# Performance work log

Measured on AMD Instinct MI355X. Metric: run time of the kernel, lower is better.

The kernel has to match this reference:

```python
import jax, jax.numpy as jnp
import numpy as np

PI = np.pi


def _apply_1q(state, gate, wire, n):
    # state: [B, 2**n] complex64; gate: [2,2] (shared) or [B,2,2] (per-sample)
    # PennyLane convention: wire 0 is the most-significant bit of the state index.
    B = state.shape[0]
    left, right = 2 ** wire, 2 ** (n - wire - 1)
    s = state.reshape(B, left, 2, right)
    if gate.ndim == 2:
        s = jnp.einsum('kl,balr->bakr', gate, s)
    else:
        s = jnp.einsum('bkl,balr->bakr', gate, s)
    return s.reshape(B, -1)


def _apply_cz(state, wire, n):
    # CZ on (wire, wire+1): flip sign of |..11..> amplitudes
    B = state.shape[0]
    left, right = 2 ** wire, 2 ** (n - wire - 2)
    s = state.reshape(B, left, 2, 2, right)
    s = s.at[:, :, 1, 1, :].multiply(-1.0)
    return s.reshape(B, -1)


def _ry_batched(theta):
    # theta: [B] -> [B,2,2] complex RY(theta)
    h = 0.5 * theta
    c, s = jnp.cos(h), jnp.sin(h)
    g = jnp.stack([jnp.stack([c, -s], -1), jnp.stack([s, c], -1)], -2)
    return g.astype(jnp.complex64)


def _rot(phi, theta, omega):
    # Rot = RZ(omega) @ RY(theta) @ RZ(phi)
    c, s = jnp.cos(0.5 * theta), jnp.sin(0.5 * theta)
    e_mm = jnp.exp(-0.5j * (phi + omega))
    e_pm = jnp.exp(0.5j * (phi - omega))
    e_mp = jnp.exp(-0.5j * (phi - omega))
    e_pp = jnp.exp(0.5j * (phi + omega))
    g = jnp.stack([jnp.stack([e_mm * c, -e_pm * s]), jnp.stack([e_mp * s, e_pp * c])])
    return g.astype(jnp.complex64)


def _simulate(enc, weights):
    # enc: [B, n_qubits] in [-1,1]; weights: [n_layers, n_qubits, 3]
    n_layers, n, _ = weights.shape
    B = enc.shape[0]
    state = jnp.zeros((B, 2 ** n), jnp.complex64).at[:, 0].set(1.0)
    ry = [_ry_batched(enc[:, i] * PI) for i in range(n)]
    for l in range(n_layers):
        for i in range(n):
            state = _apply_1q(state, ry[i], i, n)
        for i in range(n):
            state = _apply_1q(state, _rot(weights[l, i, 0], weights[l, i, 1], weights[l, i, 2]), i, n)
        for i in range(n - 1):
            state = _apply_cz(state, i, n)
    for i in range(n):
        state = _apply_1q(state, ry[i], i, n)
    probs = state.real ** 2 + state.imag ** 2  # [B, 2**n]
    # <Z_i> = sum_k probs[k] * (-1)^bit_i(k), wire 0 = MSB
    bits = (jnp.arange(2 ** n)[None, :] >> (n - 1 - jnp.arange(n))[:, None]) & 1
    signs = (1 - 2 * bits).astype(probs.dtype)  # [n, 2**n]
    return probs @ signs.T  # [B, n]


def setup_inputs() -> dict:
    B, D, NQ, NL, NA = 32768, 16, 8, 4, 4
    key = jax.random.key(0)
    ks = jax.random.split(key, 6)

    def lin(k, o, i):
        b = 1.0 / np.sqrt(i)
        k1, k2 = jax.random.split(k)
        return (jax.random.uniform(k1, (o, i), jnp.float32, -b, b),
                jax.random.uniform(k2, (o,), jnp.float32, -b, b))

    enc_w1, enc_b1 = lin(ks[1], 8, D)
    enc_w2, enc_b2 = lin(ks[2], NQ, 8)
    dec_w1, dec_b1 = lin(ks[3], 8, NQ)
    dec_w2, dec_b2 = lin(ks[4], NA, 8)
    q_weights = jax.random.uniform(ks[5], (NL, NQ, 3), jnp.float32, 0.0, 2.0 * PI)
    x = jax.random.normal(ks[0], (B, D), jnp.float32)
    return {"x": x, "enc_w1": enc_w1, "enc_b1": enc_b1, "enc_w2": enc_w2, "enc_b2": enc_b2,
            "q_weights": q_weights, "dec_w1": dec_w1, "dec_b1": dec_b1, "dec_w2": dec_w2, "dec_b2": dec_b2}


def reference(x, enc_w1, enc_b1, enc_w2, enc_b2, q_weights, dec_w1, dec_b1, dec_w2, dec_b2):
    h = jax.nn.relu(x @ enc_w1.T + enc_b1)
    enc = jnp.tanh(h @ enc_w2.T + enc_b2)          # [B, n_qubits]
    q = _simulate(enc, q_weights)                  # [B, n_qubits] PauliZ expvals
    h2 = jax.nn.relu(q @ dec_w1.T + dec_b1)
    return h2 @ dec_w2.T + dec_b2                  # [B, n_actions]
```

## Files before the change

kernel.cpp:

```cpp
#include <hip/hip_runtime.h>
#include <math.h>


#define PI_F 3.14159265358979323846f

struct C2 { float re, im; };

__device__ __forceinline__ C2 cmul(C2 a, C2 b) {
    C2 r;
    r.re = fmaf(a.re, b.re, -a.im * b.im);
    r.im = fmaf(a.re, b.im,  a.im * b.re);
    return r;
}

__device__ __forceinline__ void cdot2(const C2& g, float ar, float ai,
                                      const C2& h, float br, float bi,
                                      float& outr, float& outi) {
    outr = fmaf(g.re, ar, fmaf(-g.im, ai, fmaf(h.re, br, -h.im * bi)));
    outi = fmaf(g.re, ai, fmaf( g.im, ar, fmaf(h.re, bi,  h.im * br)));
}

__device__ __forceinline__ void load_G(const float* __restrict__ c_lds, int g,
                                       float cc, float ss,
                                       C2& G00, C2& G01, C2& G10, C2& G11) {
    const float4* cp = (const float4*)(c_lds + 8 * g);
    float4 c0 = cp[0];
    float4 c1 = cp[1];
    G00.re = fmaf(c0.x, cc,  c0.z * ss);  G00.im = fmaf(c0.y, cc,  c0.w * ss);
    G01.re = fmaf(c0.z, cc, -c0.x * ss);  G01.im = fmaf(c0.w, cc, -c0.y * ss);
    G10.re = fmaf(c1.x, cc,  c1.z * ss);  G10.im = fmaf(c1.y, cc,  c1.w * ss);
    G11.re = fmaf(c1.z, cc, -c1.x * ss);  G11.im = fmaf(c1.w, cc, -c1.y * ss);
}

__device__ __forceinline__ void apply_gate16(int q, int lane,
                                             C2 G00, C2 G01, C2 G10, C2 G11,
                                             float sr[16], float si[16]) {
    if (q < 4) {
        const int sh = 3 - q;
        const int m = 1 << sh;
        const bool hi = (lane >> sh) & 1;
        C2 cS = hi ? G11 : G00;
        C2 cO = hi ? G10 : G01;
#pragma unroll
        for (int t = 0; t < 16; t++) {
            float pr = __shfl_xor(sr[t], m, 64);
            float pi = __shfl_xor(si[t], m, 64);
            float nr, ni;
            cdot2(cS, sr[t], si[t], cO, pr, pi, nr, ni);
            sr[t] = nr; si[t] = ni;
        }
    } else {
        const int st = 1 << (7 - q);
#pragma unroll
        for (int t = 0; t < 16; t++) {
            if ((t & st) == 0) {
                const int u = t + st;
                float ar = sr[t], ai = si[t], br = sr[u], bi = si[u];
                cdot2(G00, ar, ai, G01, br, bi, sr[t], si[t]);
                cdot2(G10, ar, ai, G11, br, bi, sr[u], si[u]);
            }
        }
    }
}

__device__ __constant__ const bool CZNEG[16] =
    { false,false,false,true,  false,false,true,false,
      false,false,false,true,  true, true, false,true };

__global__ __launch_bounds__(256) void qdqn_kernel(
    const float* __restrict__ x,
    const float* __restrict__ ew1, const float* __restrict__ eb1,
    const float* __restrict__ ew2, const float* __restrict__ eb2,
    const float* __restrict__ qw,
    const float* __restrict__ dw1, const float* __restrict__ db1,
    const float* __restrict__ dw2, const float* __restrict__ db2,
    float* __restrict__ out, int B, int NL) {
    __shared__ __align__(16) float c_lds[64 * 8];

    const int tid = threadIdx.x;
    const int n_gates = NL * 8;

    if (tid < n_gates) {
        const int g = tid;
        float phi = qw[3 * g + 0], th = qw[3 * g + 1], om = qw[3 * g + 2];
        float c = __cosf(0.5f * th), s = __sinf(0.5f * th);
        float A = 0.5f * (phi + om), Bb = 0.5f * (phi - om);
        float cA = __cosf(A), sA = __sinf(A), cB = __cosf(Bb), sB = __sinf(Bb);
        float* o = c_lds + 8 * g;
        o[0] =  cA * c;  o[1] = -sA * c;
        o[2] = -cB * s;  o[3] = -sB * s;
        o[4] =  cB * s;  o[5] = -sB * s;
        o[6] =  cA * c;  o[7] =  sA * c;
    }
    __syncthreads();

    const int wave = tid >> 6;
    const int lane = tid & 63;
    const int L = lane & 15;
    int s = (blockIdx.x * 4 + wave) * 4 + (lane >> 4);
    if (s >= B) s = B - 1;

    float xv[16];
    const float4* xp = (const float4*)(x + s * 16);
#pragma unroll
    for (int i = 0; i < 4; i++) {
        float4 v = xp[i];
        xv[4*i] = v.x; xv[4*i+1] = v.y; xv[4*i+2] = v.z; xv[4*i+3] = v.w;
    }
    float hbuf[8];
#pragma unroll
    for (int j = 0; j < 8; j++) {
        float a = eb1[j];
#pragma unroll
        for (int i = 0; i < 16; i++) a = fmaf(ew1[j * 16 + i], xv[i], a);
        hbuf[j] = fmaxf(a, 0.0f);
    }
    float cq[8], sq[8];
#pragma unroll
    for (int q = 0; q < 8; q++) {
        float a = eb2[q];
#pragma unroll
        for (int j = 0; j < 8; j++) a = fmaf(ew2[q * 8 + j], hbuf[j], a);
        float e = 1.0f - __fdividef(2.0f, __expf(2.0f * a) + 1.0f);
        float ang = e * (0.5f * PI_F);
        cq[q] = __cosf(ang);
        sq[q] = __sinf(ang);
    }

    {
    }
    const int L0 = L & 1, L1b = (L >> 1) & 1, L2b = (L >> 2) & 1, L3b = (L >> 3) & 1;
    const int cnt = (L3b & L2b) + (L2b & L1b) + (L1b & L0);
    const float mL = (cnt & 1) ? -1.0f : 1.0f;
    const float mH = L0 ? -mL : mL;

    float sr[16], si[16];
    {
        C2 P; P.re = 1.0f; P.im = 0.0f;
        C2 F[4][2];
#pragma unroll
        for (int q = 0; q < 8; q++) {
            C2 G00, G01, G10, G11;
            load_G(c_lds, q, cq[q], sq[q], G00, G01, G10, G11);
            if (q < 4) {
                const int sh = 3 - q;
                const bool hi = (lane >> sh) & 1;
                C2 f = hi ? G10 : G00;
                P = cmul(P, f);
            } else {
                F[q - 4][0] = G00;
                F[q - 4][1] = G10;
            }
        }
        C2 A0 = cmul(P, F[0][0]), A1 = cmul(P, F[0][1]);
        C2 Bv[4];
        Bv[0] = cmul(A0, F[1][0]); Bv[1] = cmul(A0, F[1][1]);
        Bv[2] = cmul(A1, F[1][0]); Bv[3] = cmul(A1, F[1][1]);
        C2 Cv[8];
#pragma unroll
        for (int i = 0; i < 8; i++) Cv[i] = cmul(Bv[i >> 1], F[2][i & 1]);
#pragma unroll
        for (int t = 0; t < 16; t++) {
            C2 v = cmul(Cv[t >> 1], F[3][t & 1]);
            float m = (t < 8) ? mL : mH;
            m = CZNEG[t] ? -m : m;
            sr[t] = v.re * m;
            si[t] = v.im * m;
        }
    }

    for (int l = 1; l < NL; l++) {
#pragma unroll
        for (int q = 0; q < 8; q++) {
            C2 G00, G01, G10, G11;
            load_G(c_lds, l * 8 + q, cq[q], sq[q], G00, G01, G10, G11);
            apply_gate16(q, lane, G00, G01, G10, G11, sr, si);
        }
#pragma unroll
        for (int t = 0; t < 16; t++) {
            float m = (t < 8) ? mL : mH;
            m = CZNEG[t] ? -m : m;
            sr[t] *= m; si[t] *= m;
        }
    }

#pragma unroll
    for (int q = 0; q < 8; q++) {
        const float c = cq[q], sv = sq[q];
        if (q < 4) {
            const int sh = 3 - q;
            const int m = 1 << sh;
            const bool hi = (lane >> sh) & 1;
            const float cO = hi ? sv : -sv;
#pragma unroll
            for (int t = 0; t < 16; t++) {
                float pr = __shfl_xor(sr[t], m, 64);
                float pi = __shfl_xor(si[t], m, 64);
                sr[t] = fmaf(c, sr[t], cO * pr);
                si[t] = fmaf(c, si[t], cO * pi);
            }
        } else {
            const int st = 1 << (7 - q);
#pragma unroll
            for (int t = 0; t < 16; t++) {
                if ((t & st) == 0) {
                    const int u = t + st;
                    float ar = sr[t], ai = si[t], br = sr[u], bi = si[u];
                    sr[t] = fmaf(c, ar, -sv * br); si[t] = fmaf(c, ai, -sv * bi);
                    sr[u] = fmaf(sv, ar,  c * br); si[u] = fmaf(sv, ai,  c * bi);
                }
            }
        }
    }

    float p[16];
#pragma unroll
    for (int t = 0; t < 16; t++) p[t] = fmaf(sr[t], sr[t], si[t] * si[t]);

    float e0 = p[0]+p[1],  e1 = p[2]+p[3],  e2 = p[4]+p[5],  e3 = p[6]+p[7];
    float e4 = p[8]+p[9],  e5 = p[10]+p[11], e6 = p[12]+p[13], e7 = p[14]+p[15];
    float q0 = e0+e1, q1 = e2+e3, q2 = e4+e5, q3 = e6+e7;
    float h0 = q0+q1, h1 = q2+q3;
    float sumP = h0 + h1;

    float z[8];
#pragma unroll
    for (int w = 0; w < 4; w++)
        z[w] = ((L >> (3 - w)) & 1) ? -sumP : sumP;
    z[4] = h0 - h1;
    z[5] = (q0 - q1) + (q2 - q3);
    z[6] = (e0 - e1) + (e2 - e3) + (e4 - e5) + (e6 - e7);
    z[7] = (p[0]-p[1]) + (p[2]-p[3]) + (p[4]-p[5]) + (p[6]-p[7])
         + (p[8]-p[9]) + (p[10]-p[11]) + (p[12]-p[13]) + (p[14]-p[15]);

#pragma unroll
    for (int m = 1; m < 16; m <<= 1) {
#pragma unroll
        for (int w = 0; w < 8; w++) z[w] += __shfl_xor(z[w], m, 64);
    }

    float h2[8];
#pragma unroll
    for (int j = 0; j < 8; j++) {
        float a = db1[j];
#pragma unroll
        for (int w = 0; w < 8; w++) a = fmaf(dw1[j * 8 + w], z[w], a);
        h2[j] = fmaxf(a, 0.0f);
    }
    if (L < 4) {
        float a = db2[L];
#pragma unroll
        for (int j = 0; j < 8; j++) a = fmaf(dw2[L * 8 + j], h2[j], a);
        out[s * 4 + L] = a;
    }
}

extern "C" void kernel_launch(void* const* d_in, const int* in_sizes, int n_in,
                              void* d_out, int out_size, void* d_ws, size_t ws_size,
                              hipStream_t stream) {
    const float* x   = (const float*)d_in[0];
    const float* ew1 = (const float*)d_in[1];
    const float* eb1 = (const float*)d_in[2];
    const float* ew2 = (const float*)d_in[3];
    const float* eb2 = (const float*)d_in[4];
    const float* qw  = (const float*)d_in[5];
    const float* dw1 = (const float*)d_in[6];
    const float* db1 = (const float*)d_in[7];
    const float* dw2 = (const float*)d_in[8];
    const float* db2 = (const float*)d_in[9];
    float* out = (float*)d_out;

    int B = in_sizes[0] / 16;
    int n_gates = in_sizes[5] / 3;
    int NL = n_gates / 8;

    int blocks = (B + 15) / 16;
    qdqn_kernel<<<blocks, 256, 0, stream>>>(x, ew1, eb1, ew2, eb2, qw,
                                            dw1, db1, dw2, db2, out, B, NL);
}
```

Measured before the change: 139.0 us.

## Use DPP/swizzle lane exchanges, compact gate coefficients, one-wave blocks

Cross-lane butterfly exchanges switch from __shfl_xor (ds_bpermute) to DPP quad/row moves and ds_swizzle, covering the lane-xor distances 1, 2, 4 and 8. The fused gate is stored as two complex coefficients, using the unitary structure, and the per-lane conjugate selection becomes sign-bit XOR masks, which cuts LDS traffic and selects. Blocks shrink from four waves to a single 64-thread wave, each block precomputing the gate table on its own. This removes shuffle latency and LDS pressure but adds redundant per-block precompute and four times as many blocks.

New measurement: 137.1 us. About the same (-1.4%).

```diff
diff --git a/kernel.cpp b/kernel.cpp
--- a/kernel.cpp
+++ b/kernel.cpp
@@ -13,61 +13,90 @@
     return r;
 }
 
-__device__ __forceinline__ void cdot2(const C2& g, float ar, float ai,
-                                      const C2& h, float br, float bi,
-                                      float& outr, float& outi) {
-    outr = fmaf(g.re, ar, fmaf(-g.im, ai, fmaf(h.re, br, -h.im * bi)));
-    outi = fmaf(g.re, ai, fmaf( g.im, ar, fmaf(h.re, bi,  h.im * br)));
-}
-
-__device__ __forceinline__ void load_G(const float* __restrict__ c_lds, int g,
-                                       float cc, float ss,
-                                       C2& G00, C2& G01, C2& G10, C2& G11) {
-    const float4* cp = (const float4*)(c_lds + 8 * g);
-    float4 c0 = cp[0];
-    float4 c1 = cp[1];
-    G00.re = fmaf(c0.x, cc,  c0.z * ss);  G00.im = fmaf(c0.y, cc,  c0.w * ss);
-    G01.re = fmaf(c0.z, cc, -c0.x * ss);  G01.im = fmaf(c0.w, cc, -c0.y * ss);
-    G10.re = fmaf(c1.x, cc,  c1.z * ss);  G10.im = fmaf(c1.y, cc,  c1.w * ss);
-    G11.re = fmaf(c1.z, cc, -c1.x * ss);  G11.im = fmaf(c1.w, cc, -c1.y * ss);
-}
-
-__device__ __forceinline__ void apply_gate16(int q, int lane,
-                                             C2 G00, C2 G01, C2 G10, C2 G11,
-                                             float sr[16], float si[16]) {
-    if (q < 4) {
-        const int sh = 3 - q;
-        const int m = 1 << sh;
-        const bool hi = (lane >> sh) & 1;
-        C2 cS = hi ? G11 : G00;
-        C2 cO = hi ? G10 : G01;
-#pragma unroll
-        for (int t = 0; t < 16; t++) {
-            float pr = __shfl_xor(sr[t], m, 64);
-            float pi = __shfl_xor(si[t], m, 64);
-            float nr, ni;
-            cdot2(cS, sr[t], si[t], cO, pr, pi, nr, ni);
-            sr[t] = nr; si[t] = ni;
-        }
-    } else {
-        const int st = 1 << (7 - q);
-#pragma unroll
-        for (int t = 0; t < 16; t++) {
-            if ((t & st) == 0) {
-                const int u = t + st;
-                float ar = sr[t], ai = si[t], br = sr[u], bi = si[u];
-                cdot2(G00, ar, ai, G01, br, bi, sr[t], si[t]);
-                cdot2(G10, ar, ai, G11, br, bi, sr[u], si[u]);
-            }
-        }
-    }
-}
-
-__device__ __constant__ const bool CZNEG[16] =
-    { false,false,false,true,  false,false,true,false,
-      false,false,false,true,  true, true, false,true };
-
-__global__ __launch_bounds__(256) void qdqn_kernel(
+__device__ __forceinline__ float fxor(float x, int m) {
+    return __int_as_float(__float_as_int(x) ^ m);
+}
+
+template<int CTRL>
+__device__ __forceinline__ float dppf(float x) {
+    int xi = __float_as_int(x);
+    int r = __builtin_amdgcn_update_dpp(xi, xi, CTRL, 0xF, 0xF, false);
+    return __int_as_float(r);
+}
+__device__ __forceinline__ float swz4(float x) {
+    return __int_as_float(__builtin_amdgcn_ds_swizzle(__float_as_int(x), 0x101F));
+}
+template<int M>
+__device__ __forceinline__ float lxor(float x) {
+    if constexpr (M == 1)      return dppf<0xB1>(x);
+    else if constexpr (M == 2) return dppf<0x4E>(x);
+    else if constexpr (M == 4) return swz4(x);
+    else                       return dppf<0x128>(x);
+}
+
+template<int M>
+__device__ __forceinline__ void cross_gate(float cSr, float cSi, float cOr, float cOi,
+                                           float sr[16], float si[16]) {
+#pragma unroll
+    for (int t = 0; t < 16; t++) {
+        float pr = lxor<M>(sr[t]);
+        float pi = lxor<M>(si[t]);
+        float nr = fmaf(cSr, sr[t], fmaf(-cSi, si[t], fmaf(cOr, pr, -cOi * pi)));
+        float ni = fmaf(cSr, si[t], fmaf( cSi, sr[t], fmaf(cOr, pi,  cOi * pr)));
+        sr[t] = nr; si[t] = ni;
+    }
+}
+
+template<int ST>
+__device__ __forceinline__ void inlane_gate(float ar, float ai, float br, float bi,
+                                            float sr[16], float si[16]) {
+#pragma unroll
+    for (int t = 0; t < 16; t++) {
+        if ((t & ST) == 0) {
+            const int u = t + ST;
+            float xr = sr[t], xi = si[t], yr = sr[u], yi = si[u];
+            sr[t] = fmaf(ar, xr, fmaf(-ai, xi, fmaf(-br, yr, -bi * yi)));
+            si[t] = fmaf(ar, xi, fmaf( ai, xr, fmaf(-br, yi,  bi * yr)));
+            sr[u] = fmaf(br, xr, fmaf(-bi, xi, fmaf( ar, yr,  ai * yi)));
+            si[u] = fmaf(br, xi, fmaf( bi, xr, fmaf( ar, yi, -ai * yr)));
+        }
+    }
+}
+
+template<int M>
+__device__ __forceinline__ void cross_ry(float c, float cO, float sr[16], float si[16]) {
+#pragma unroll
+    for (int t = 0; t < 16; t++) {
+        float pr = lxor<M>(sr[t]);
+        float pi = lxor<M>(si[t]);
+        sr[t] = fmaf(c, sr[t], cO * pr);
+        si[t] = fmaf(c, si[t], cO * pi);
+    }
+}
+template<int ST>
+__device__ __forceinline__ void inlane_ry(float c, float s, float sr[16], float si[16]) {
+#pragma unroll
+    for (int t = 0; t < 16; t++) {
+        if ((t & ST) == 0) {
+            const int u = t + ST;
+            float xr = sr[t], xi = si[t], yr = sr[u], yi = si[u];
+            sr[t] = fmaf(c, xr, -s * yr); si[t] = fmaf(c, xi, -s * yi);
+            sr[u] = fmaf(s, xr,  c * yr); si[u] = fmaf(s, xi,  c * yi);
+        }
+    }
+}
+
+__device__ __forceinline__ void load_G2(const float* __restrict__ c_lds, int g,
+                                        float cc, float ss,
+                                        float& ar, float& ai, float& br, float& bi) {
+    const float4 c0 = *(const float4*)(c_lds + 4 * g);
+    ar = fmaf(c0.x, cc, -c0.z * ss);
+    ai = fmaf(c0.y, cc,  c0.w * ss);
+    br = fmaf(c0.z, cc,  c0.x * ss);
+    bi = fmaf(c0.w, cc, -c0.y * ss);
+}
+
+__global__ __launch_bounds__(64) void qdqn_kernel(
     const float* __restrict__ x,
     const float* __restrict__ ew1, const float* __restrict__ eb1,
     const float* __restrict__ ew2, const float* __restrict__ eb2,
@@ -75,29 +104,24 @@
     const float* __restrict__ dw1, const float* __restrict__ db1,
     const float* __restrict__ dw2, const float* __restrict__ db2,
     float* __restrict__ out, int B, int NL) {
-    __shared__ __align__(16) float c_lds[64 * 8];
-
-    const int tid = threadIdx.x;
+    __shared__ __align__(16) float c_lds[32 * 4];
+
+    const int lane = threadIdx.x;
     const int n_gates = NL * 8;
 
-    if (tid < n_gates) {
-        const int g = tid;
+    if (lane < n_gates) {
+        const int g = lane;
         float phi = qw[3 * g + 0], th = qw[3 * g + 1], om = qw[3 * g + 2];
         float c = __cosf(0.5f * th), s = __sinf(0.5f * th);
         float A = 0.5f * (phi + om), Bb = 0.5f * (phi - om);
-        float cA = __cosf(A), sA = __sinf(A), cB = __cosf(Bb), sB = __sinf(Bb);
-        float* o = c_lds + 8 * g;
-        o[0] =  cA * c;  o[1] = -sA * c;
-        o[2] = -cB * s;  o[3] = -sB * s;
-        o[4] =  cB * s;  o[5] = -sB * s;
-        o[6] =  cA * c;  o[7] =  sA * c;
+        float* o = c_lds + 4 * g;
+        o[0] =  __cosf(A) * c;  o[1] = -__sinf(A) * c;
+        o[2] =  __cosf(Bb) * s; o[3] = -__sinf(Bb) * s;
     }
     __syncthreads();
 
-    const int wave = tid >> 6;
-    const int lane = tid & 63;
     const int L = lane & 15;
-    int s = (blockIdx.x * 4 + wave) * 4 + (lane >> 4);
+    int s = blockIdx.x * 4 + (lane >> 4);
     if (s >= B) s = B - 1;
 
     float xv[16];
@@ -127,12 +151,21 @@
         sq[q] = __sinf(ang);
     }
 
-    {
-    }
+    int hiM[4], loM[4];
+#pragma unroll
+    for (int q = 0; q < 4; q++) {
+        int hi = (L >> (3 - q)) & 1;
+        hiM[q] = hi << 31;
+        loM[q] = hiM[q] ^ 0x80000000;
+    }
+
     const int L0 = L & 1, L1b = (L >> 1) & 1, L2b = (L >> 2) & 1, L3b = (L >> 3) & 1;
     const int cnt = (L3b & L2b) + (L2b & L1b) + (L1b & L0);
     const float mL = (cnt & 1) ? -1.0f : 1.0f;
     const float mH = L0 ? -mL : mL;
+    constexpr bool CZNEG[16] =
+        { false,false,false,true,  false,false,true,false,
+          false,false,false,true,  true, true, false,true };
 
     float sr[16], si[16];
     {
@@ -140,16 +173,15 @@
         C2 F[4][2];
 #pragma unroll
         for (int q = 0; q < 8; q++) {
-            C2 G00, G01, G10, G11;
-            load_G(c_lds, q, cq[q], sq[q], G00, G01, G10, G11);
+            float ar, ai, br, bi;
+            load_G2(c_lds, q, cq[q], sq[q], ar, ai, br, bi);
             if (q < 4) {
-                const int sh = 3 - q;
-                const bool hi = (lane >> sh) & 1;
-                C2 f = hi ? G10 : G00;
+                const bool hi = (L >> (3 - q)) & 1;
+                C2 f; f.re = hi ? br : ar; f.im = hi ? bi : ai;
                 P = cmul(P, f);
             } else {
-                F[q - 4][0] = G00;
-                F[q - 4][1] = G10;
+                F[q-4][0].re = ar; F[q-4][0].im = ai;
+                F[q-4][1].re = br; F[q-4][1].im = bi;
             }
         }
         C2 A0 = cmul(P, F[0][0]), A1 = cmul(P, F[0][1]);
@@ -170,12 +202,24 @@
     }
 
     for (int l = 1; l < NL; l++) {
-#pragma unroll
-        for (int q = 0; q < 8; q++) {
-            C2 G00, G01, G10, G11;
-            load_G(c_lds, l * 8 + q, cq[q], sq[q], G00, G01, G10, G11);
-            apply_gate16(q, lane, G00, G01, G10, G11, sr, si);
-        }
+        const int g0 = l * 8;
+        float ar, ai, br, bi;
+        load_G2(c_lds, g0 + 0, cq[0], sq[0], ar, ai, br, bi);
+        cross_gate<8>(ar, fxor(ai, hiM[0]), fxor(br, loM[0]), bi, sr, si);
+        load_G2(c_lds, g0 + 1, cq[1], sq[1], ar, ai, br, bi);
+        cross_gate<4>(ar, fxor(ai, hiM[1]), fxor(br, loM[1]), bi, sr, si);
+        load_G2(c_lds, g0 + 2, cq[2], sq[2], ar, ai, br, bi);
+        cross_gate<2>(ar, fxor(ai, hiM[2]), fxor(br, loM[2]), bi, sr, si);
+        load_G2(c_lds, g0 + 3, cq[3], sq[3], ar, ai, br, bi);
+        cross_gate<1>(ar, fxor(ai, hiM[3]), fxor(br, loM[3]), bi, sr, si);
+        load_G2(c_lds, g0 + 4, cq[4], sq[4], ar, ai, br, bi);
+        inlane_gate<8>(ar, ai, br, bi, sr, si);
+        load_G2(c_lds, g0 + 5, cq[5], sq[5], ar, ai, br, bi);
+        inlane_gate<4>(ar, ai, br, bi, sr, si);
+        load_G2(c_lds, g0 + 6, cq[6], sq[6], ar, ai, br, bi);
+        inlane_gate<2>(ar, ai, br, bi, sr, si);
+        load_G2(c_lds, g0 + 7, cq[7], sq[7], ar, ai, br, bi);
+        inlane_gate<1>(ar, ai, br, bi, sr, si);
 #pragma unroll
         for (int t = 0; t < 16; t++) {
             float m = (t < 8) ? mL : mH;
@@ -184,34 +228,14 @@
         }
     }
 
-#pragma unroll
-    for (int q = 0; q < 8; q++) {
-        const float c = cq[q], sv = sq[q];
-        if (q < 4) {
-            const int sh = 3 - q;
-            const int m = 1 << sh;
-            const bool hi = (lane >> sh) & 1;
-            const float cO = hi ? sv : -sv;
-#pragma unroll
-            for (int t = 0; t < 16; t++) {
-                float pr = __shfl_xor(sr[t], m, 64);
-                float pi = __shfl_xor(si[t], m, 64);
-                sr[t] = fmaf(c, sr[t], cO * pr);
-                si[t] = fmaf(c, si[t], cO * pi);
-            }
-        } else {
-            const int st = 1 << (7 - q);
-#pragma unroll
-            for (int t = 0; t < 16; t++) {
-                if ((t & st) == 0) {
-                    const int u = t + st;
-                    float ar = sr[t], ai = si[t], br = sr[u], bi = si[u];
-                    sr[t] = fmaf(c, ar, -sv * br); si[t] = fmaf(c, ai, -sv * bi);
-                    sr[u] = fmaf(sv, ar,  c * br); si[u] = fmaf(sv, ai,  c * bi);
-                }
-            }
-        }
-    }
+    cross_ry<8>(cq[0], fxor(sq[0], loM[0]), sr, si);
+    cross_ry<4>(cq[1], fxor(sq[1], loM[1]), sr, si);
+    cross_ry<2>(cq[2], fxor(sq[2], loM[2]), sr, si);
+    cross_ry<1>(cq[3], fxor(sq[3], loM[3]), sr, si);
+    inlane_ry<8>(cq[4], sq[4], sr, si);
+    inlane_ry<4>(cq[5], sq[5], sr, si);
+    inlane_ry<2>(cq[6], sq[6], sr, si);
+    inlane_ry<1>(cq[7], sq[7], sr, si);
 
     float p[16];
 #pragma unroll
@@ -234,10 +258,13 @@
          + (p[8]-p[9]) + (p[10]-p[11]) + (p[12]-p[13]) + (p[14]-p[15]);
 
 #pragma unroll
-    for (int m = 1; m < 16; m <<= 1) {
-#pragma unroll
-        for (int w = 0; w < 8; w++) z[w] += __shfl_xor(z[w], m, 64);
-    }
+    for (int w = 0; w < 8; w++) z[w] += lxor<1>(z[w]);
+#pragma unroll
+    for (int w = 0; w < 8; w++) z[w] += lxor<2>(z[w]);
+#pragma unroll
+    for (int w = 0; w < 8; w++) z[w] += lxor<4>(z[w]);
+#pragma unroll
+    for (int w = 0; w < 8; w++) z[w] += lxor<8>(z[w]);
 
     float h2[8];
 #pragma unroll
@@ -274,7 +301,7 @@
     int n_gates = in_sizes[5] / 3;
     int NL = n_gates / 8;
 
-    int blocks = (B + 15) / 16;
-    qdqn_kernel<<<blocks, 256, 0, stream>>>(x, ew1, eb1, ew2, eb2, qw,
-                                            dw1, db1, dw2, db2, out, B, NL);
-}
+    int blocks = (B + 3) / 4;
+    qdqn_kernel<<<blocks, 64, 0, stream>>>(x, ew1, eb1, ew2, eb2, qw,
+                                           dw1, db1, dw2, db2, out, B, NL);
+}
```
